# Optimization experiments

Measured on AMD Instinct MI355X. Metric: run time of the kernel, lower is better.

The kernel has to match this reference:

```python
import jax, jax.numpy as jnp
import numpy as np

N_BITS = 8          # MULTIPLIER_N_BITS in MCT
SIGNED = True
THRESHOLD = 2.0
EPS = 1e-8
N_CLUSTERS = 16


def setup_inputs() -> dict:
    key = jax.random.key(0)
    kx, kc = jax.random.split(key)
    x = jax.random.normal(kx, (32, 128, 56, 56), dtype=jnp.float32)
    # integer-valued cluster centers inside the signed 8-bit range, as in MCT's LUT kmeans
    centers = jnp.sort(
        jax.random.randint(kc, (N_CLUSTERS,), -(2 ** (N_BITS - 1)), 2 ** (N_BITS - 1) - 1)
    ).astype(jnp.float32)
    return {"x": x, "cluster_centers": centers}


def reference(x, cluster_centers):
    signed = int(SIGNED)
    scale = 2.0 ** (N_BITS - signed)            # 128 for signed
    clip_max = 2 ** (N_BITS - 1) - 1 if SIGNED else 2 ** N_BITS - 1
    clip_min = -(2 ** (N_BITS - 1)) if SIGNED else 0
    # 1) scale into the 8-bit range and clip
    t = jnp.clip(x / (THRESHOLD + EPS) * scale, clip_min, clip_max)
    # 2) nearest cluster center (broadcast [..., 1] vs [K])
    assignments = jnp.argmin(jnp.abs(t[..., None] - cluster_centers), axis=-1)
    centers = cluster_centers[assignments]
    # 3) scale back to the original range
    return centers / scale * THRESHOLD
```

## Files before the change

### kernel.cpp

```cpp
#include <hip/hip_runtime.h>

#define NCLUST 16

__global__ __launch_bounds__(256) void lut_fakequant_kernel(
    const float* __restrict__ x,
    const float* __restrict__ centers,
    float* __restrict__ out,
    int n4, int tail, long long tail_base)
{
    float c[NCLUST];
#pragma unroll
    for (int k = 0; k < NCLUST; ++k) c[k] = centers[k];

    const int i = blockIdx.x * blockDim.x + threadIdx.x;

    if (i < n4) {
        const float4* __restrict__ x4 = (const float4*)x;
        float4* __restrict__ o4 = (float4*)out;
        float4 v = x4[i];
        float in[4] = {v.x, v.y, v.z, v.w};
        float res[4];
#pragma unroll
        for (int e = 0; e < 4; ++e) {
            float t = in[e] * 64.0f;
            t = fminf(fmaxf(t, -128.0f), 127.0f);
            float best  = c[0];
            float bestd = __builtin_fabsf(t - c[0]);
#pragma unroll
            for (int k = 1; k < NCLUST; ++k) {
                float d = __builtin_fabsf(t - c[k]);
                bool lt = d < bestd;
                best  = lt ? c[k] : best;
                bestd = fminf(d, bestd);
            }
            res[e] = best * 0.015625f;
        }
        o4[i] = make_float4(res[0], res[1], res[2], res[3]);
    }

    if (i < tail) {
        float t = x[tail_base + i] * 64.0f;
        t = fminf(fmaxf(t, -128.0f), 127.0f);
        float best  = c[0];
        float bestd = __builtin_fabsf(t - c[0]);
#pragma unroll
        for (int k = 1; k < NCLUST; ++k) {
            float d = __builtin_fabsf(t - c[k]);
            bool lt = d < bestd;
            best  = lt ? c[k] : best;
            bestd = fminf(d, bestd);
        }
        out[tail_base + i] = best * 0.015625f;
    }
}

extern "C" void kernel_launch(void* const* d_in, const int* in_sizes, int n_in,
                              void* d_out, int out_size, void* d_ws, size_t ws_size,
                              hipStream_t stream) {
    const float* x       = (const float*)d_in[0];
    const float* centers = (const float*)d_in[1];
    float* out           = (float*)d_out;

    const int n    = in_sizes[0];
    const int n4   = n / 4;
    const int tail = n - n4 * 4;
    const long long tail_base = (long long)n4 * 4;

    const int block = 256;
    const int grid  = (n4 + block - 1) / block;

    lut_fakequant_kernel<<<grid, block, 0, stream>>>(x, centers, out, n4, tail, tail_base);
}
```

Baseline: 106.4 us.

## Replace 16-way nearest-center search with precomputed shared-memory bucket table

Builds a 512-entry table on device mapping half-unit buckets of the clipped value to the two bracketing cluster centers. The main kernel loads it into LDS and resolves each element with one lookup and two distance compares instead of scanning all 16 centers. Each thread now processes two float4s. This adds an extra kernel launch, a per-block table load and barrier, and possible LDS bank conflicts.

```diff
diff --git a/kernel.cpp b/kernel.cpp
--- a/kernel.cpp
+++ b/kernel.cpp
@@ -1,56 +1,75 @@
 #include <hip/hip_runtime.h>
 
 #define NCLUST 16
+#define TBL 512
+#define EPT 8
+
+__global__ __launch_bounds__(512) void build_table_kernel(
+    const float* __restrict__ centers, float2* __restrict__ tbl)
+{
+    int b = threadIdx.x;
+    float c[NCLUST];
+#pragma unroll
+    for (int k = 0; k < NCLUST; ++k) c[k] = centers[k];
+    int cnt = 0;
+#pragma unroll
+    for (int k = 0; k < NCLUST; ++k)
+        cnt += (fmaf(c[k], 2.0f, 256.0f) <= (float)b) ? 1 : 0;
+    int j = cnt - 1;
+    j = j < 0 ? 0 : (j > NCLUST - 2 ? NCLUST - 2 : j);
+    tbl[b] = make_float2(c[j], c[j + 1]);
+}
+
+__device__ __forceinline__ float quant1(float xv, const float2* __restrict__ lut)
+{
+    float t = xv * 64.0f;
+    t = fminf(fmaxf(t, -128.0f), 127.0f);
+    float s = fmaf(t, 2.0f, 256.0f);
+    int b = (int)s;
+    float2 p = lut[b];
+    float d0 = __builtin_fabsf(t - p.x);
+    float d1 = __builtin_fabsf(t - p.y);
+    return (d0 <= d1 ? p.x : p.y) * 0.015625f;
+}
 
 __global__ __launch_bounds__(256) void lut_fakequant_kernel(
     const float* __restrict__ x,
-    const float* __restrict__ centers,
+    const float2* __restrict__ tbl,
     float* __restrict__ out,
-    int n4, int tail, long long tail_base)
+    int n4, int tail)
 {
-    float c[NCLUST];
-#pragma unroll
-    for (int k = 0; k < NCLUST; ++k) c[k] = centers[k];
+    __shared__ __align__(16) float2 lut[TBL];
+    ((float4*)lut)[threadIdx.x] = ((const float4*)tbl)[threadIdx.x];
+    __syncthreads();
 
-    const int i = blockIdx.x * blockDim.x + threadIdx.x;
+    const float4* __restrict__ x4 = (const float4*)x;
+    float4* __restrict__ o4 = (float4*)out;
 
-    if (i < n4) {
-        const float4* __restrict__ x4 = (const float4*)x;
-        float4* __restrict__ o4 = (float4*)out;
-        float4 v = x4[i];
-        float in[4] = {v.x, v.y, v.z, v.w};
-        float res[4];
-#pragma unroll
-        for (int e = 0; e < 4; ++e) {
-            float t = in[e] * 64.0f;
-            t = fminf(fmaxf(t, -128.0f), 127.0f);
-            float best  = c[0];
-            float bestd = __builtin_fabsf(t - c[0]);
-#pragma unroll
-            for (int k = 1; k < NCLUST; ++k) {
-                float d = __builtin_fabsf(t - c[k]);
-                bool lt = d < bestd;
-                best  = lt ? c[k] : best;
-                bestd = fminf(d, bestd);
-            }
-            res[e] = best * 0.015625f;
-        }
-        o4[i] = make_float4(res[0], res[1], res[2], res[3]);
+    const int i0 = blockIdx.x * (256 * EPT / 4) + threadIdx.x;
+    const int i1 = i0 + 256;
+    const bool g0 = i0 < n4;
+    const bool g1 = i1 < n4;
+
+    float4 v0, v1;
+    if (g0) v0 = x4[i0];
+    if (g1) v1 = x4[i1];
+
+    if (g0) {
+        float4 r;
+        r.x = quant1(v0.x, lut); r.y = quant1(v0.y, lut);
+        r.z = quant1(v0.z, lut); r.w = quant1(v0.w, lut);
+        o4[i0] = r;
+    }
+    if (g1) {
+        float4 r;
+        r.x = quant1(v1.x, lut); r.y = quant1(v1.y, lut);
+        r.z = quant1(v1.z, lut); r.w = quant1(v1.w, lut);
+        o4[i1] = r;
     }
 
-    if (i < tail) {
-        float t = x[tail_base + i] * 64.0f;
-        t = fminf(fmaxf(t, -128.0f), 127.0f);
-        float best  = c[0];
-        float bestd = __builtin_fabsf(t - c[0]);
-#pragma unroll
-        for (int k = 1; k < NCLUST; ++k) {
-            float d = __builtin_fabsf(t - c[k]);
-            bool lt = d < bestd;
-            best  = lt ? c[k] : best;
-            bestd = fminf(d, bestd);
-        }
-        out[tail_base + i] = best * 0.015625f;
+    if (blockIdx.x == 0 && threadIdx.x < tail) {
+        long long idx = (long long)n4 * 4 + threadIdx.x;
+        out[idx] = quant1(x[idx], lut);
     }
 }
 
@@ -60,14 +79,15 @@
     const float* x       = (const float*)d_in[0];
     const float* centers = (const float*)d_in[1];
     float* out           = (float*)d_out;
+    float2* tbl          = (float2*)d_ws;
 
     const int n    = in_sizes[0];
     const int n4   = n / 4;
     const int tail = n - n4 * 4;
-    const long long tail_base = (long long)n4 * 4;
 
-    const int block = 256;
-    const int grid  = (n4 + block - 1) / block;
+    build_table_kernel<<<1, TBL, 0, stream>>>(centers, tbl);
 
-    lut_fakequant_kernel<<<grid, block, 0, stream>>>(x, centers, out, n4, tail, tail_base);
+    const int f4_per_block = 256 * EPT / 4;
+    const int grid = (n4 + f4_per_block - 1) / f4_per_block;
+    lut_fakequant_kernel<<<grid, 256, 0, stream>>>(x, tbl, out, n4, tail);
 }
```

After: 102.2 us. 3.9% less time.
